# Optimization experiments

Hardware: AMD Instinct MI355X
Metric: run time of the kernel (lower is better)

The kernel has to match this reference:

```python
import jax, jax.numpy as jnp
import numpy as np

NEG_SLOPE = 0.01
BN_EPS = 1e-5
H1, C1 = 4, 32   # layer 1: heads, out_channels
H2, C2 = 4, 64   # layer 2
G, P = 2048, 18  # graphs, nodes per graph
N = G * P


def _glorot(key, shape):
    fan_in, fan_out = shape[0], shape[1]
    lim = float(np.sqrt(6.0 / (fan_in + fan_out)))
    return jax.random.uniform(key, shape, jnp.float32, -lim, lim)


def setup_inputs() -> dict:
    key = jax.random.key(0)
    ks = jax.random.split(key, 24)
    # block-diagonal fully-connected directed graphs (no self loops)
    idx = np.arange(P)
    s, d = np.meshgrid(idx, idx, indexing='ij')
    m = s != d
    s, d = s[m], d[m]                      # 306 edges per graph
    off = (np.arange(G) * P)[:, None]
    src = (off + s[None, :]).reshape(-1)
    dst = (off + d[None, :]).reshape(-1)
    edge_index = jnp.asarray(np.stack([src, dst]), dtype=jnp.int32)
    batch = jnp.repeat(jnp.arange(G, dtype=jnp.int32), P)
    E = edge_index.shape[1]
    inp = {
        'x': jax.random.normal(ks[0], (N, 6), jnp.float32),
        'edge_attr': jax.random.uniform(ks[1], (E, 1), jnp.float32),
        'edge_index': edge_index,
        'batch': batch,
        # GATv2 layer 1 (in=6 -> H1*C1=128)
        'W1l': _glorot(ks[2], (6, H1 * C1)), 'b1l': jnp.zeros((H1 * C1,)),
        'W1r': _glorot(ks[3], (6, H1 * C1)), 'b1r': jnp.zeros((H1 * C1,)),
        'We1': _glorot(ks[4], (1, H1 * C1)),
        'att1': _glorot(ks[5], (H1, C1)),
        'bias1': jnp.zeros((H1 * C1,)),
        # GATv2 layer 2 (in=128 -> H2*C2=256)
        'W2l': _glorot(ks[6], (H1 * C1, H2 * C2)), 'b2l': jnp.zeros((H2 * C2,)),
        'W2r': _glorot(ks[7], (H1 * C1, H2 * C2)), 'b2r': jnp.zeros((H2 * C2,)),
        'We2': _glorot(ks[8], (1, H2 * C2)),
        'att2': _glorot(ks[9], (H2, C2)),
        'bias2': jnp.zeros((H2 * C2,)),
        # batch norms
        'g1': jnp.ones((H1 * C1,)), 'be1': jnp.zeros((H1 * C1,)),
        'g2': jnp.ones((H2 * C2,)), 'be2': jnp.zeros((H2 * C2,)),
        # MLP head
        'Wfc1': _glorot(ks[10], (H2 * C2, 512)), 'bfc1': jnp.zeros((512,)),
        'Wfc2': _glorot(ks[11], (512, 128)), 'bfc2': jnp.zeros((128,)),
        'Wfc3': _glorot(ks[12], (128, 1)), 'bfc3': jnp.zeros((1,)),
    }
    return inp


def _lrelu(x, slope=NEG_SLOPE):
    return jnp.where(x > 0, x, slope * x)


def _gatv2(x, src, dst, eattr, Wl, bl, Wr, br, We, att, bout, H, C):
    n = x.shape[0]
    xl = (x @ Wl + bl).reshape(n, H, C)   # source projection (lin_l)
    xr = (x @ Wr + br).reshape(n, H, C)   # target projection (lin_r)
    ee = (eattr @ We).reshape(-1, H, C)   # edge projection (lin_edge)
    m = _lrelu(xl[src] + xr[dst] + ee)    # [E,H,C]
    alpha = jnp.einsum('ehc,hc->eh', m, att)
    amax = jax.ops.segment_max(alpha, dst, num_segments=n)
    ea = jnp.exp(alpha - amax[dst])
    denom = jax.ops.segment_sum(ea, dst, num_segments=n)
    a = ea / (denom[dst] + 1e-16)
    out = jax.ops.segment_sum(xl[src] * a[..., None], dst, num_segments=n)
    return out.reshape(n, H * C) + bout


def _bn(h, g, b):
    mu = h.mean(0)
    var = ((h - mu) ** 2).mean(0)
    return g * (h - mu) * jax.lax.rsqrt(var + BN_EPS) + b


def _add_self_loops(src, dst, eattr, n):
    # PyG fill_value='mean': self-loop attr = mean of incoming edge attrs
    loop = jnp.arange(n, dtype=src.dtype)
    s = jax.ops.segment_sum(eattr, dst, num_segments=n)
    c = jax.ops.segment_sum(jnp.ones((eattr.shape[0], 1), eattr.dtype), dst, num_segments=n)
    loop_attr = s / jnp.maximum(c, 1.0)
    return (jnp.concatenate([src, loop]), jnp.concatenate([dst, loop]),
            jnp.concatenate([eattr, loop_attr], axis=0))


def reference(x, edge_attr, edge_index, batch,
              W1l, b1l, W1r, b1r, We1, att1, bias1,
              W2l, b2l, W2r, b2r, We2, att2, bias2,
              g1, be1, g2, be2,
              Wfc1, bfc1, Wfc2, bfc2, Wfc3, bfc3):
    src, dst = edge_index[0], edge_index[1]
    src, dst, ea = _add_self_loops(src, dst, edge_attr, x.shape[0])
    h = _gatv2(x, src, dst, ea, W1l, b1l, W1r, b1r, We1, att1, bias1, H1, C1)
    h = _lrelu(_bn(h, g1, be1))
    h = _gatv2(h, src, dst, ea, W2l, b2l, W2r, b2r, We2, att2, bias2, H2, C2)
    h = _lrelu(_bn(h, g2, be2))
    # global mean pool over graphs
    num_g = G
    s = jax.ops.segment_sum(h, batch, num_segments=num_g)
    c = jax.ops.segment_sum(jnp.ones((h.shape[0], 1), h.dtype), batch, num_segments=num_g)
    h = s / jnp.maximum(c, 1.0)
    h = _lrelu(h @ Wfc1 + bfc1)
    h = _lrelu(h @ Wfc2 + bfc2)
    return h @ Wfc3 + bfc3
```

## Files before the change

kernel.cpp:

```cpp
#include <hip/hip_runtime.h>
#include <cstddef>

#define GG 2048
#define PP 18
#define NNODE (GG*PP)
#define EPG 306
#define F1 128
#define F2 256
#define ASX 20
#define INF 6
#define HP1 36
#define XR1 144
#define HPR1 20
#define XRR1 80
#define HP2 68
#define XR2 272
#define HPP 36
#define XRP 144

typedef unsigned short u16;
typedef unsigned int u32;
typedef __attribute__((ext_vector_type(8))) short short8;
typedef __attribute__((ext_vector_type(4))) float f32x4;

__device__ __forceinline__ float lrelu(float v) { return fmaxf(v, 0.01f*v); }

__device__ __forceinline__ u16 f2b(float x) {
    union { float f; unsigned u; } c; c.f = x;
    unsigned r = c.u + 0x7FFF + ((c.u >> 16) & 1);
    return (u16)(r >> 16);
}
__device__ __forceinline__ float b2f(u16 v) {
    union { unsigned u; float f; } c; c.u = ((unsigned)v) << 16;
    return c.f;
}
__device__ __forceinline__ float bpk_lo(u32 u) { return __uint_as_float(u << 16); }
__device__ __forceinline__ float bpk_hi(u32 u) { return __uint_as_float(u & 0xffff0000u); }

__global__ __launch_bounds__(256) void gat1_kernel(
    const float* __restrict__ x, const float* __restrict__ eattr,
    const float* __restrict__ W1l, const float* __restrict__ b1l,
    const float* __restrict__ W1r, const float* __restrict__ b1r,
    const float* __restrict__ We1, const float* __restrict__ att1,
    const float* __restrict__ bias1, float* __restrict__ h1,
    float* __restrict__ sum1, float* __restrict__ ss1)
{
    __shared__ float xs[PP*INF];
    __shared__ float wl[INF*F1], wr[INF*F1];
    __shared__ float bl[F1], br[F1];
    __shared__ float2 wa1[4*HP1];
    __shared__ float ea[PP*PP];
    __shared__ float xl[PP*XR1];
    __shared__ u32 xrp1[PP*XRR1];
    __shared__ float alpha[PP*4*ASX];
    const int g = blockIdx.x, tid = threadIdx.x;

    if (tid < PP*INF) xs[tid] = x[g*PP*INF + tid];
    for (int i = tid; i < INF*F1; i += 256) { wl[i] = W1l[i]; wr[i] = W1r[i]; }
    if (tid < F1) {
        bl[tid] = b1l[tid]; br[tid] = b1r[tid];
        int off = (tid >> 5)*HP1 + (tid & 31);
        wa1[off] = make_float2(We1[tid], att1[tid]);
    }
    for (int t = tid; t < EPG; t += 256) {
        int s = t/17, pos = t%17;
        int d = pos + (pos >= s);
        ea[s*PP + d] = eattr[g*EPG + t];
    }
    __syncthreads();
    if (tid < PP) {
        float sum = 0.f;
        for (int s = 0; s < PP; ++s) if (s != tid) sum += ea[s*PP + tid];
        ea[tid*PP + tid] = sum * (1.f/17.f);
    }
    __syncthreads();
    {
        u16* xr16 = (u16*)xrp1;
        for (int o = tid; o < PP*F1; o += 256) {
            int n = o >> 7, j = o & (F1-1);
            float al = bl[j], ar = br[j];
            #pragma unroll
            for (int k = 0; k < INF; ++k) {
                float xv = xs[n*INF + k];
                al = fmaf(xv, wl[k*F1 + j], al);
                ar = fmaf(xv, wr[k*F1 + j], ar);
            }
            xl[n*XR1 + (j >> 5)*HP1 + (j & 31)] = al;
            xr16[n*(2*XRR1) + (j >> 5)*(2*HPR1) + (j & 31)] = f2b(ar);
        }
    }
    __syncthreads();
    {
        const int h = tid & 3, u = tid >> 2;
        const int s = u % PP, q = u / PP;
        if (q < 3) {
            const int d0 = q*6;
            const float* xlrow = &xl[s*XR1 + h*HP1];
            const u32*  xrb    = &xrp1[d0*XRR1 + h*HPR1];
            float e[6];
            #pragma unroll
            for (int dd = 0; dd < 6; ++dd) e[dd] = ea[s*PP + d0 + dd];
            float acc[6] = {0,0,0,0,0,0};
            #pragma unroll
            for (int ch = 0; ch < 4; ++ch) {
                const int cc = ch*8, cp = ch*4;
                float4 xla = *(const float4*)&xlrow[cc];
                float4 xlb = *(const float4*)&xlrow[cc + 4];
                float4 wa01 = *(const float4*)&wa1[h*HP1 + cc];
                float4 wa23 = *(const float4*)&wa1[h*HP1 + cc + 2];
                float4 wa45 = *(const float4*)&wa1[h*HP1 + cc + 4];
                float4 wa67 = *(const float4*)&wa1[h*HP1 + cc + 6];
                #pragma unroll
                for (int dd = 0; dd < 6; ++dd) {
                    uint4 xru = *(const uint4*)&xrb[dd*XRR1 + cp];
                    float ev = e[dd];
                    float v0 = fmaf(ev, wa01.x, xla.x + bpk_lo(xru.x)); v0 = fmaxf(v0, 0.01f*v0);
                    float v1 = fmaf(ev, wa01.z, xla.y + bpk_hi(xru.x)); v1 = fmaxf(v1, 0.01f*v1);
                    float v2 = fmaf(ev, wa23.x, xla.z + bpk_lo(xru.y)); v2 = fmaxf(v2, 0.01f*v2);
                    float v3 = fmaf(ev, wa23.z, xla.w + bpk_hi(xru.y)); v3 = fmaxf(v3, 0.01f*v3);
                    float v4 = fmaf(ev, wa45.x, xlb.x + bpk_lo(xru.z)); v4 = fmaxf(v4, 0.01f*v4);
                    float v5 = fmaf(ev, wa45.z, xlb.y + bpk_hi(xru.z)); v5 = fmaxf(v5, 0.01f*v5);
                    float v6 = fmaf(ev, wa67.x, xlb.z + bpk_lo(xru.w)); v6 = fmaxf(v6, 0.01f*v6);
                    float v7 = fmaf(ev, wa67.z, xlb.w + bpk_hi(xru.w)); v7 = fmaxf(v7, 0.01f*v7);
                    float a01 = fmaf(v0, wa01.y, v1*wa01.w);
                    float a23 = fmaf(v2, wa23.y, v3*wa23.w);
                    float a45 = fmaf(v4, wa45.y, v5*wa45.w);
                    float a67 = fmaf(v6, wa67.y, v7*wa67.w);
                    acc[dd] += (a01 + a23) + (a45 + a67);
                }
            }
            #pragma unroll
            for (int dd = 0; dd < 6; ++dd)
                alpha[((d0 + dd)*4 + h)*ASX + s] = acc[dd];
        }
    }
    __syncthreads();
    if (tid < PP*4) {
        float* a = &alpha[tid*ASX];
        float m = -1e30f;
        for (int s = 0; s < PP; ++s) m = fmaxf(m, a[s]);
        float sum = 0.f;
        for (int s = 0; s < PP; ++s) sum += __expf(a[s] - m);
        float inv = 1.f/(sum + 1e-16f);
        for (int s = 0; s < PP; ++s) a[s] = __expf(a[s] - m) * inv;
    }
    __syncthreads();
    float s_loc = 0.f, q_loc = 0.f;
    {
        const int j = tid & 127, h = j >> 5, c = j & 31, d0 = tid >> 7;
        float xlc[PP];
        #pragma unroll
        for (int s = 0; s < PP; ++s) xlc[s] = xl[s*XR1 + h*HP1 + c];
        const float bv = bias1[j];
        #pragma unroll
        for (int k = 0; k < 9; ++k) {
            int d = d0 + 2*k;
            const float* ap = &alpha[(d*4 + h)*ASX];
            float4 a0 = *(const float4*)&ap[0];
            float4 a1 = *(const float4*)&ap[4];
            float4 a2 = *(const float4*)&ap[8];
            float4 a3 = *(const float4*)&ap[12];
            float acc = bv;
            acc = fmaf(a0.x, xlc[0],  acc); acc = fmaf(a0.y, xlc[1],  acc);
            acc = fmaf(a0.z, xlc[2],  acc); acc = fmaf(a0.w, xlc[3],  acc);
            acc = fmaf(a1.x, xlc[4],  acc); acc = fmaf(a1.y, xlc[5],  acc);
            acc = fmaf(a1.z, xlc[6],  acc); acc = fmaf(a1.w, xlc[7],  acc);
            acc = fmaf(a2.x, xlc[8],  acc); acc = fmaf(a2.y, xlc[9],  acc);
            acc = fmaf(a2.z, xlc[10], acc); acc = fmaf(a2.w, xlc[11], acc);
            acc = fmaf(a3.x, xlc[12], acc); acc = fmaf(a3.y, xlc[13], acc);
            acc = fmaf(a3.z, xlc[14], acc); acc = fmaf(a3.w, xlc[15], acc);
            acc = fmaf(ap[16], xlc[16], acc); acc = fmaf(ap[17], xlc[17], acc);
            h1[(size_t)g*(PP*F1) + d*F1 + j] = acc;
            s_loc += acc;
            q_loc = fmaf(acc, acc, q_loc);
        }
    }
    __syncthreads();
    wl[tid] = s_loc;
    wr[tid] = q_loc;
    __syncthreads();
    if (tid < F1) {
        atomicAdd(&sum1[tid], wl[tid] + wl[tid + 128]);
        atomicAdd(&ss1[tid],  wr[tid] + wr[tid + 128]);
    }
}

__global__ void prep_w(const float* __restrict__ W2l, const float* __restrict__ W2r,
                       const float* __restrict__ b2l, const float* __restrict__ b2r,
                       u16* __restrict__ wbt, float* __restrict__ biascat,
                       float* __restrict__ st)
{
    int t = blockIdx.x*blockDim.x + threadIdx.x;
    if (t < 1536) st[t] = 0.f;
    if (t < 512*128) {
        int c = t >> 7, k = t & 127;
        float v = (c < 256) ? W2l[k*256 + c] : W2r[k*256 + (c-256)];
        wbt[t] = f2b(v);
    } else if (t < 512*128 + 512) {
        int c = t - 512*128;
        biascat[c] = (c < 256) ? b2l[c] : b2r[c-256];
    }
}

__global__ __launch_bounds__(256) void gemm2_kernel(
    const float* __restrict__ h1,
    const float* __restrict__ sum1, const float* __restrict__ ss1,
    const float* __restrict__ g1, const float* __restrict__ be1,
    const u16* __restrict__ wbt, const float* __restrict__ biascat, u16* __restrict__ xlr)
{
    __shared__ u16 As[64*128];
    __shared__ u16 Bs[64*128];
    __shared__ float scs[F1], shs[F1];
    const int b = blockIdx.x;
    const int bm = b >> 3, bn = b & 7;
    const int r0 = bm*64, c0 = bn*64;
    const int tid = threadIdx.x;

    if (tid < F1) {
        float mu = sum1[tid] * (1.f/NNODE);
        float var = ss1[tid] * (1.f/NNODE) - mu*mu;
        float s = g1[tid] * rsqrtf(var + 1e-5f);
        scs[tid] = s; shs[tid] = be1[tid] - mu*s;
    }
    __syncthreads();
    for (int i = tid*8; i < 64*128; i += 256*8) {
        int r = i >> 7, c = i & 127;
        float4 v0 = *(const float4*)&h1[(size_t)(r0+r)*128 + c];
        float4 v1 = *(const float4*)&h1[(size_t)(r0+r)*128 + c + 4];
        short8 a;
        a[0] = (short)f2b(lrelu(fmaf(scs[c+0], v0.x, shs[c+0])));
        a[1] = (short)f2b(lrelu(fmaf(scs[c+1], v0.y, shs[c+1])));
        a[2] = (short)f2b(lrelu(fmaf(scs[c+2], v0.z, shs[c+2])));
        a[3] = (short)f2b(lrelu(fmaf(scs[c+3], v0.w, shs[c+3])));
        a[4] = (short)f2b(lrelu(fmaf(scs[c+4], v1.x, shs[c+4])));
        a[5] = (short)f2b(lrelu(fmaf(scs[c+5], v1.y, shs[c+5])));
        a[6] = (short)f2b(lrelu(fmaf(scs[c+6], v1.z, shs[c+6])));
        a[7] = (short)f2b(lrelu(fmaf(scs[c+7], v1.w, shs[c+7])));
        int idx = i ^ ((r & 7) << 3);
        *reinterpret_cast<short8*>(&As[idx]) = a;
        *reinterpret_cast<short8*>(&Bs[idx]) =
            *reinterpret_cast<const short8*>(&wbt[(size_t)(c0+r)*128 + c]);
    }
    __syncthreads();

    const int w = tid >> 6, l = tid & 63;
    const int lr = l & 15, lk = (l >> 4) * 8;
    const int ar = w*16 + lr;
    f32x4 acc[4] = {f32x4{0,0,0,0}, f32x4{0,0,0,0}, f32x4{0,0,0,0}, f32x4{0,0,0,0}};

    #pragma unroll
    for (int kk = 0; kk < 4; ++kk) {
        int k0 = kk*32 + lk;
        short8 a = *reinterpret_cast<const short8*>(&As[(ar*128 + k0) ^ ((ar & 7) << 3)]);
        #pragma unroll
        for (int n = 0; n < 4; ++n) {
            int br = n*16 + lr;
            short8 bf = *reinterpret_cast<const short8*>(&Bs[(br*128 + k0) ^ ((br & 7) << 3)]);
            acc[n] = __builtin_amdgcn_mfma_f32_16x16x32_bf16(a, bf, acc[n], 0, 0, 0);
        }
    }
    const int rbase = r0 + w*16 + (l >> 4)*4;
    #pragma unroll
    for (int n = 0; n < 4; ++n) {
        int C = c0 + n*16 + lr;
        float bv = biascat[C];
        #pragma unroll
        for (int j = 0; j < 4; ++j) {
            xlr[(size_t)(rbase + j)*512 + C] = f2b(acc[n][j] + bv);
        }
    }
}

__global__ __launch_bounds__(256) void gat2_attn(
    const u16* __restrict__ xlr, const float* __restrict__ eattr,
    const float* __restrict__ We2, const float* __restrict__ att2,
    const float* __restrict__ bias2, float* __restrict__ h2,
    float* __restrict__ sum2, float* __restrict__ ss2)
{
    __shared__ float xl[PP*XR2];
    __shared__ u32 xrp[PP*XRP];
    __shared__ float ea[PP*PP];
    __shared__ float alpha[PP*4*ASX];
    __shared__ float2 wa2[4*HP2];
    const int g = blockIdx.x, tid = threadIdx.x;

    {
        int off = (tid >> 6)*HP2 + (tid & 63);
        wa2[off] = make_float2(We2[tid], att2[tid]);
    }
    for (int i4 = tid; i4 < PP*128; i4 += 256) {
        int i = i4*4, n = i >> 9, j = i & 511;
        const u16* src = &xlr[(size_t)(g*PP + n)*512 + j];
        if (j < 256) {
            ushort4 v = *reinterpret_cast<const ushort4*>(src);
            int off = n*XR2 + (j >> 6)*HP2 + (j & 63);
            *(float4*)&xl[off] = make_float4(b2f(v.x), b2f(v.y), b2f(v.z), b2f(v.w));
        } else {
            uint2 p = *reinterpret_cast<const uint2*>(src);
            int j2 = j & 255;
            int off = n*XRP + (j2 >> 6)*HPP + ((j2 & 63) >> 1);
            *(uint2*)&xrp[off] = p;
        }
    }
    for (int t = tid; t < EPG; t += 256) {
        int s = t/17, pos = t%17;
        int d = pos + (pos >= s);
        ea[s*PP + d] = eattr[g*EPG + t];
    }
    __syncthreads();
    if (tid < PP) {
        float sum = 0.f;
        for (int s = 0; s < PP; ++s) if (s != tid) sum += ea[s*PP + tid];
        ea[tid*PP + tid] = sum * (1.f/17.f);
    }
    __syncthreads();
    {
        const int h = tid & 3, u = tid >> 2;
        const int s = u % PP, q = u / PP;
        if (q < 3) {
            const int d0 = q*6;
            const float* xlrow = &xl[s*XR2 + h*HP2];
            const u32*  xrb    = &xrp[d0*XRP + h*HPP];
            float e[6];
            #pragma unroll
            for (int dd = 0; dd < 6; ++dd) e[dd] = ea[s*PP + d0 + dd];
            float acc[6] = {0,0,0,0,0,0};
            #pragma unroll
            for (int ch = 0; ch < 8; ++ch) {
                const int cc = ch*8, cp = ch*4;
                float4 xla = *(const float4*)&xlrow[cc];
                float4 xlb = *(const float4*)&xlrow[cc + 4];
                float4 wa01 = *(const float4*)&wa2[h*HP2 + cc];
                float4 wa23 = *(const float4*)&wa2[h*HP2 + cc + 2];
                float4 wa45 = *(const float4*)&wa2[h*HP2 + cc + 4];
                float4 wa67 = *(const float4*)&wa2[h*HP2 + cc + 6];
                #pragma unroll
                for (int dd = 0; dd < 6; ++dd) {
                    uint4 xru = *(const uint4*)&xrb[dd*XRP + cp];
                    float ev = e[dd];
                    float v0 = fmaf(ev, wa01.x, xla.x + bpk_lo(xru.x)); v0 = fmaxf(v0, 0.01f*v0);
                    float v1 = fmaf(ev, wa01.z, xla.y + bpk_hi(xru.x)); v1 = fmaxf(v1, 0.01f*v1);
                    float v2 = fmaf(ev, wa23.x, xla.z + bpk_lo(xru.y)); v2 = fmaxf(v2, 0.01f*v2);
                    float v3 = fmaf(ev, wa23.z, xla.w + bpk_hi(xru.y)); v3 = fmaxf(v3, 0.01f*v3);
                    float v4 = fmaf(ev, wa45.x, xlb.x + bpk_lo(xru.z)); v4 = fmaxf(v4, 0.01f*v4);
                    float v5 = fmaf(ev, wa45.z, xlb.y + bpk_hi(xru.z)); v5 = fmaxf(v5, 0.01f*v5);
                    float v6 = fmaf(ev, wa67.x, xlb.z + bpk_lo(xru.w)); v6 = fmaxf(v6, 0.01f*v6);
                    float v7 = fmaf(ev, wa67.z, xlb.w + bpk_hi(xru.w)); v7 = fmaxf(v7, 0.01f*v7);
                    float a01 = fmaf(v0, wa01.y, v1*wa01.w);
                    float a23 = fmaf(v2, wa23.y, v3*wa23.w);
                    float a45 = fmaf(v4, wa45.y, v5*wa45.w);
                    float a67 = fmaf(v6, wa67.y, v7*wa67.w);
                    acc[dd] += (a01 + a23) + (a45 + a67);
                }
            }
            #pragma unroll
            for (int dd = 0; dd < 6; ++dd)
                alpha[((d0 + dd)*4 + h)*ASX + s] = acc[dd];
        }
    }
    __syncthreads();
    if (tid < PP*4) {
        float* a = &alpha[tid*ASX];
        float m = -1e30f;
        for (int s = 0; s < PP; ++s) m = fmaxf(m, a[s]);
        float sum = 0.f;
        for (int s = 0; s < PP; ++s) sum += __expf(a[s] - m);
        float inv = 1.f/(sum + 1e-16f);
        for (int s = 0; s < PP; ++s) a[s] = __expf(a[s] - m) * inv;
    }
    __syncthreads();
    float s_loc = 0.f, q_loc = 0.f;
    {
        const int j = tid, h = j >> 6, c = j & 63;
        float xlc[PP];
        #pragma unroll
        for (int s = 0; s < PP; ++s) xlc[s] = xl[s*XR2 + h*HP2 + c];
        const float bv = bias2[j];
        for (int d = 0; d < PP; ++d) {
            const float* ap = &alpha[(d*4 + h)*ASX];
            float4 a0 = *(const float4*)&ap[0];
            float4 a1 = *(const float4*)&ap[4];
            float4 a2 = *(const float4*)&ap[8];
            float4 a3 = *(const float4*)&ap[12];
            float acc = bv;
            acc = fmaf(a0.x, xlc[0],  acc); acc = fmaf(a0.y, xlc[1],  acc);
            acc = fmaf(a0.z, xlc[2],  acc); acc = fmaf(a0.w, xlc[3],  acc);
            acc = fmaf(a1.x, xlc[4],  acc); acc = fmaf(a1.y, xlc[5],  acc);
            acc = fmaf(a1.z, xlc[6],  acc); acc = fmaf(a1.w, xlc[7],  acc);
            acc = fmaf(a2.x, xlc[8],  acc); acc = fmaf(a2.y, xlc[9],  acc);
            acc = fmaf(a2.z, xlc[10], acc); acc = fmaf(a2.w, xlc[11], acc);
            acc = fmaf(a3.x, xlc[12], acc); acc = fmaf(a3.y, xlc[13], acc);
            acc = fmaf(a3.z, xlc[14], acc); acc = fmaf(a3.w, xlc[15], acc);
            acc = fmaf(ap[16], xlc[16], acc); acc = fmaf(ap[17], xlc[17], acc);
            h2[(size_t)g*(PP*F2) + d*F2 + j] = acc;
            s_loc += acc;
            q_loc = fmaf(acc, acc, q_loc);
        }
    }
    atomicAdd(&sum2[tid], s_loc);
    atomicAdd(&ss2[tid], q_loc);
}

__global__ __launch_bounds__(512) void mlp_kernel(
    const float* __restrict__ h2,
    const float* __restrict__ sum2, const float* __restrict__ ss2,
    const float* __restrict__ g2, const float* __restrict__ be2,
    const float* __restrict__ Wfc1, const float* __restrict__ bfc1,
    const float* __restrict__ Wfc2, const float* __restrict__ bfc2,
    const float* __restrict__ Wfc3, const float* __restrict__ bfc3,
    float* __restrict__ out)
{
    __shared__ float pooled[4][F2];
    __shared__ float y1[4][512];
    __shared__ float part[3][4][128];
    __shared__ float y2[4][128];
    const int g0 = blockIdx.x * 4, tid = threadIdx.x;
    {
        const int col = tid & 255;
        float mu = sum2[col] * (1.f/NNODE);
        float var = ss2[col] * (1.f/NNODE) - mu*mu;
        const float scv = g2[col] * rsqrtf(var + 1e-5f);
        const float shv = be2[col] - mu*scv;
        #pragma unroll
        for (int r = 0; r < 2; ++r) {
            int gi = (tid >> 8) + 2*r;
            float s = 0.f;
            #pragma unroll 3
            for (int n = 0; n < PP; ++n) {
                float v = fmaf(scv, h2[((size_t)(g0+gi)*PP + n)*F2 + col], shv);
                s += fmaxf(v, 0.01f*v);
            }
            pooled[gi][col] = s * (1.f/18.f);
        }
    }
    __syncthreads();
    {
        const int j = tid;
        float acc[4];
        float bv = bfc1[j];
        #pragma unroll
        for (int gi = 0; gi < 4; ++gi) acc[gi] = bv;
        #pragma unroll 8
        for (int k = 0; k < F2; ++k) {
            float w = Wfc1[k*512 + j];
            #pragma unroll
            for (int gi = 0; gi < 4; ++gi) acc[gi] = fmaf(pooled[gi][k], w, acc[gi]);
        }
        #pragma unroll
        for (int gi = 0; gi < 4; ++gi) y1[gi][j] = fmaxf(acc[gi], 0.01f*acc[gi]);
    }
    __syncthreads();
    {
        const int kh = tid >> 7, j = tid & 127;
        float acc[4] = {0,0,0,0};
        #pragma unroll 8
        for (int k = kh*128; k < kh*128 + 128; ++k) {
            float w = Wfc2[k*128 + j];
            #pragma unroll
            for (int gi = 0; gi < 4; ++gi) acc[gi] = fmaf(y1[gi][k], w, acc[gi]);
        }
        if (kh > 0) {
            #pragma unroll
            for (int gi = 0; gi < 4; ++gi) part[kh-1][gi][j] = acc[gi];
        }
        __syncthreads();
        if (kh == 0) {
            float w3 = Wfc3[j], bv = bfc2[j];
            #pragma unroll
            for (int gi = 0; gi < 4; ++gi) {
                float v = acc[gi] + part[0][gi][j] + part[1][gi][j] + part[2][gi][j] + bv;
                y2[gi][j] = fmaxf(v, 0.01f*v) * w3;
            }
        }
    }
    __syncthreads();
    if (tid < 256) {
        int gi = tid >> 6, lx = tid & 63;
        float p = y2[gi][lx] + y2[gi][lx + 64];
        p += __shfl_xor(p, 1); p += __shfl_xor(p, 2); p += __shfl_xor(p, 4);
        p += __shfl_xor(p, 8); p += __shfl_xor(p, 16); p += __shfl_xor(p, 32);
        if (lx == 0) out[g0 + gi] = p + bfc3[0];
    }
}

extern "C" void kernel_launch(void* const* d_in, const int* in_sizes, int n_in,
                              void* d_out, int out_size, void* d_ws, size_t ws_size,
                              hipStream_t stream)
{
    const float* x     = (const float*)d_in[0];
    const float* eattr = (const float*)d_in[1];
    const float* W1l   = (const float*)d_in[4];
    const float* b1l   = (const float*)d_in[5];
    const float* W1r   = (const float*)d_in[6];
    const float* b1r   = (const float*)d_in[7];
    const float* We1   = (const float*)d_in[8];
    const float* att1  = (const float*)d_in[9];
    const float* bias1 = (const float*)d_in[10];
    const float* W2l   = (const float*)d_in[11];
    const float* b2l   = (const float*)d_in[12];
    const float* W2r   = (const float*)d_in[13];
    const float* b2r   = (const float*)d_in[14];
    const float* We2   = (const float*)d_in[15];
    const float* att2  = (const float*)d_in[16];
    const float* bias2 = (const float*)d_in[17];
    const float* g1    = (const float*)d_in[18];
    const float* be1   = (const float*)d_in[19];
    const float* g2    = (const float*)d_in[20];
    const float* be2   = (const float*)d_in[21];
    const float* Wfc1  = (const float*)d_in[22];
    const float* bfc1  = (const float*)d_in[23];
    const float* Wfc2  = (const float*)d_in[24];
    const float* bfc2  = (const float*)d_in[25];
    const float* Wfc3  = (const float*)d_in[26];
    const float* bfc3  = (const float*)d_in[27];
    float* out = (float*)d_out;

    float* ws = (float*)d_ws;
    float* h1 = ws;
    float* h2 = h1 + (size_t)NNODE*F1;
    float* st = h2 + (size_t)NNODE*F2;
    float* biascat = st + 1536;
    u16* xlr = (u16*)(biascat + 512);
    u16* wbt = xlr + (size_t)NNODE*F2*2;

    float* sum1 = st,     *ss1 = st+128;
    float* sum2 = st+512, *ss2 = st+768;

    prep_w<<<259, 256, 0, stream>>>(W2l, W2r, b2l, b2r, wbt, biascat, st);
    gat1_kernel<<<GG, 256, 0, stream>>>(x, eattr, W1l, b1l, W1r, b1r, We1, att1, bias1, h1, sum1, ss1);
    gemm2_kernel<<<(NNODE/64)*8, 256, 0, stream>>>(h1, sum1, ss1, g1, be1, wbt, biascat, xlr);
    gat2_attn<<<GG, 256, 0, stream>>>(xlr, eattr, We2, att2, bias2, h2, sum2, ss2);
    mlp_kernel<<<GG/4, 512, 0, stream>>>(h2, sum2, ss2, g2, be2, Wfc1, bfc1, Wfc2, bfc2, Wfc3, bfc3, out);
}
```

Baseline: 204.4 us.

## Split layer-1 linear projection into separate kernel and simplify stats reduction

Moves the layer-1 x@W1l/W1r projection out of the per-graph attention kernel into a new GEMM kernel that writes bf16 projections to global memory. The attention kernel then loads these precomputed rows instead of reloading the weights and recomputing per graph. The per-block shared-memory reduction of the BN statistics is replaced with direct per-thread atomics, which doubles the atomic traffic. The split adds a kernel launch and a global round trip, and also rounds xl to bf16, where it was fp32 before.

```diff
diff --git a/kernel.cpp b/kernel.cpp
--- a/kernel.cpp
+++ b/kernel.cpp
@@ -37,30 +37,67 @@
 __device__ __forceinline__ float bpk_lo(u32 u) { return __uint_as_float(u << 16); }
 __device__ __forceinline__ float bpk_hi(u32 u) { return __uint_as_float(u & 0xffff0000u); }
 
-__global__ __launch_bounds__(256) void gat1_kernel(
-    const float* __restrict__ x, const float* __restrict__ eattr,
+__global__ __launch_bounds__(256) void gemm1_kernel(
+    const float* __restrict__ x,
     const float* __restrict__ W1l, const float* __restrict__ b1l,
     const float* __restrict__ W1r, const float* __restrict__ b1r,
+    u16* __restrict__ xlr1)
+{
+    __shared__ float xs[32*INF];
+    __shared__ float w[INF*256];
+    __shared__ float bb[256];
+    const int n0 = blockIdx.x*32, tid = threadIdx.x;
+    for (int i = tid; i < INF*256; i += 256) {
+        int k = i >> 8, j = i & 255;
+        w[i] = (j < F1) ? W1l[k*F1 + j] : W1r[k*F1 + (j - F1)];
+    }
+    if (tid < 32*INF) xs[tid] = x[(size_t)n0*INF + tid];
+    bb[tid] = (tid < F1) ? b1l[tid] : b1r[tid - F1];
+    __syncthreads();
+    const int j = tid;
+    float wreg[INF];
+    #pragma unroll
+    for (int k = 0; k < INF; ++k) wreg[k] = w[k*256 + j];
+    const float bv = bb[j];
+    #pragma unroll 4
+    for (int n = 0; n < 32; ++n) {
+        float acc = bv;
+        #pragma unroll
+        for (int k = 0; k < INF; ++k) acc = fmaf(xs[n*INF + k], wreg[k], acc);
+        xlr1[(size_t)(n0 + n)*256 + j] = f2b(acc);
+    }
+}
+
+__global__ __launch_bounds__(256) void gat1_kernel(
+    const u16* __restrict__ xlr1, const float* __restrict__ eattr,
     const float* __restrict__ We1, const float* __restrict__ att1,
     const float* __restrict__ bias1, float* __restrict__ h1,
     float* __restrict__ sum1, float* __restrict__ ss1)
 {
-    __shared__ float xs[PP*INF];
-    __shared__ float wl[INF*F1], wr[INF*F1];
-    __shared__ float bl[F1], br[F1];
-    __shared__ float2 wa1[4*HP1];
-    __shared__ float ea[PP*PP];
     __shared__ float xl[PP*XR1];
     __shared__ u32 xrp1[PP*XRR1];
+    __shared__ float ea[PP*PP];
     __shared__ float alpha[PP*4*ASX];
+    __shared__ float2 wa1[4*HP1];
     const int g = blockIdx.x, tid = threadIdx.x;
 
-    if (tid < PP*INF) xs[tid] = x[g*PP*INF + tid];
-    for (int i = tid; i < INF*F1; i += 256) { wl[i] = W1l[i]; wr[i] = W1r[i]; }
     if (tid < F1) {
-        bl[tid] = b1l[tid]; br[tid] = b1r[tid];
         int off = (tid >> 5)*HP1 + (tid & 31);
         wa1[off] = make_float2(We1[tid], att1[tid]);
+    }
+    for (int i4 = tid; i4 < PP*64; i4 += 256) {
+        int n = i4 >> 6, jj = (i4 & 63)*4;
+        const u16* src = &xlr1[(size_t)(g*PP + n)*256 + jj];
+        if (jj < F1) {
+            ushort4 v = *reinterpret_cast<const ushort4*>(src);
+            int off = n*XR1 + (jj >> 5)*HP1 + (jj & 31);
+            *(float4*)&xl[off] = make_float4(b2f(v.x), b2f(v.y), b2f(v.z), b2f(v.w));
+        } else {
+            uint2 p = *reinterpret_cast<const uint2*>(src);
+            int j2 = jj - F1;
+            int off = n*XRR1 + (j2 >> 5)*HPR1 + ((j2 & 31) >> 1);
+            *(uint2*)&xrp1[off] = p;
+        }
     }
     for (int t = tid; t < EPG; t += 256) {
         int s = t/17, pos = t%17;
@@ -72,22 +109,6 @@
         float sum = 0.f;
         for (int s = 0; s < PP; ++s) if (s != tid) sum += ea[s*PP + tid];
         ea[tid*PP + tid] = sum * (1.f/17.f);
-    }
-    __syncthreads();
-    {
-        u16* xr16 = (u16*)xrp1;
-        for (int o = tid; o < PP*F1; o += 256) {
-            int n = o >> 7, j = o & (F1-1);
-            float al = bl[j], ar = br[j];
-            #pragma unroll
-            for (int k = 0; k < INF; ++k) {
-                float xv = xs[n*INF + k];
-                al = fmaf(xv, wl[k*F1 + j], al);
-                ar = fmaf(xv, wr[k*F1 + j], ar);
-            }
-            xl[n*XR1 + (j >> 5)*HP1 + (j & 31)] = al;
-            xr16[n*(2*XRR1) + (j >> 5)*(2*HPR1) + (j & 31)] = f2b(ar);
-        }
     }
     __syncthreads();
     {
@@ -175,14 +196,8 @@
             q_loc = fmaf(acc, acc, q_loc);
         }
     }
-    __syncthreads();
-    wl[tid] = s_loc;
-    wr[tid] = q_loc;
-    __syncthreads();
-    if (tid < F1) {
-        atomicAdd(&sum1[tid], wl[tid] + wl[tid + 128]);
-        atomicAdd(&ss1[tid],  wr[tid] + wr[tid + 128]);
-    }
+    atomicAdd(&sum1[tid & 127], s_loc);
+    atomicAdd(&ss1[tid & 127], q_loc);
 }
 
 __global__ void prep_w(const float* __restrict__ W2l, const float* __restrict__ W2r,
@@ -522,12 +537,14 @@
     float* biascat = st + 1536;
     u16* xlr = (u16*)(biascat + 512);
     u16* wbt = xlr + (size_t)NNODE*F2*2;
+    u16* xlr1 = wbt + (size_t)512*128;
 
     float* sum1 = st,     *ss1 = st+128;
     float* sum2 = st+512, *ss2 = st+768;
 
     prep_w<<<259, 256, 0, stream>>>(W2l, W2r, b2l, b2r, wbt, biascat, st);
-    gat1_kernel<<<GG, 256, 0, stream>>>(x, eattr, W1l, b1l, W1r, b1r, We1, att1, bias1, h1, sum1, ss1);
+    gemm1_kernel<<<NNODE/32, 256, 0, stream>>>(x, W1l, b1l, W1r, b1r, xlr1);
+    gat1_kernel<<<GG, 256, 0, stream>>>(xlr1, eattr, We1, att1, bias1, h1, sum1, ss1);
     gemm2_kernel<<<(NNODE/64)*8, 256, 0, stream>>>(h1, sum1, ss1, g1, be1, wbt, biascat, xlr);
     gat2_attn<<<GG, 256, 0, stream>>>(xlr, eattr, We2, att2, bias2, h2, sum2, ss2);
     mlp_kernel<<<GG/4, 512, 0, stream>>>(h2, sum2, ss2, g2, be2, Wfc1, bfc1, Wfc2, bfc2, Wfc3, bfc3, out);
```

New measurement: 258.5 us. +26.5%, slower.
